# Kernel optimization log

Measured on AMD Instinct MI355X. Metric: run time of the kernel, lower is better.

Reference implementation:

```python
import math
import jax, jax.numpy as jnp
import numpy as np

B, S, HID = 2, 1024, 2048
H, D, R = 16, 128, 64            # heads, head_dim, rope_dim_per_head
KVC, QC = 512, 1536              # kv / query compressed dims
MAX_POS = 4096


def _lin(x, w, b):
    return x @ w.T + b


def _rotate_half(x):
    x1, x2 = x[..., : x.shape[-1] // 2], x[..., x.shape[-1] // 2 :]
    return jnp.concatenate([-x2, x1], axis=-1)


def _rope_tables(dim, end, theta=10000.0):
    freqs = 1.0 / (theta ** (jnp.arange(0, dim, 2)[: dim // 2].astype(jnp.float32) / dim))
    f = jnp.outer(jnp.arange(end, dtype=jnp.float32), freqs)  # [end, dim//2]
    cos, sin = jnp.cos(f), jnp.sin(f)
    # duplicate halves so tables broadcast against the full rope dim (standard HF convention)
    return jnp.concatenate([cos, cos], -1), jnp.concatenate([sin, sin], -1)


def setup_inputs() -> dict:
    key = jax.random.key(0)
    ks = jax.random.split(key, 17)
    w = lambda k, shape: (jax.random.normal(k, shape, jnp.float32) * 0.02)
    return {
        "hidden_states": jax.random.normal(ks[0], (B, S, HID), jnp.float32),
        "W_DKV_w": w(ks[1], (KVC, HID)),  "W_DKV_b": w(ks[2], (KVC,)),
        "W_UK_w":  w(ks[3], (H * D, KVC)), "W_UK_b":  w(ks[4], (H * D,)),
        "W_UV_w":  w(ks[5], (H * D, KVC)), "W_UV_b":  w(ks[6], (H * D,)),
        "W_KR_w":  w(ks[7], (R, D)),       "W_KR_b":  w(ks[8], (R,)),
        "W_DQ_w":  w(ks[9], (QC, HID)),    "W_DQ_b":  w(ks[10], (QC,)),
        "W_UQ_w":  w(ks[11], (H * D, QC)), "W_UQ_b":  w(ks[12], (H * D,)),
        "W_QR_w":  w(ks[13], (R, D)),      "W_QR_b":  w(ks[14], (R,)),
        "W_O_w":   w(ks[15], (HID, H * D)),"W_O_b":   w(ks[16], (HID,)),
    }


def reference(hidden_states, W_DKV_w, W_DKV_b, W_UK_w, W_UK_b, W_UV_w, W_UV_b,
              W_KR_w, W_KR_b, W_DQ_w, W_DQ_b, W_UQ_w, W_UQ_b,
              W_QR_w, W_QR_b, W_O_w, W_O_b):
    b, s = hidden_states.shape[:2]
    # latent KV compression + decompression
    c_kv = _lin(hidden_states, W_DKV_w, W_DKV_b)                      # [B,S,KVC]
    k = _lin(c_kv, W_UK_w, W_UK_b).reshape(b, s, H, D)
    v = _lin(c_kv, W_UV_w, W_UV_b).reshape(b, s, H, D)
    # latent Q compression + decompression
    c_q = _lin(hidden_states, W_DQ_w, W_DQ_b)                         # [B,S,QC]
    q = _lin(c_q, W_UQ_w, W_UQ_b).reshape(b, s, H, D)
    # decoupled rope sub-dims
    k_r = _lin(k, W_KR_w, W_KR_b)                                     # [B,S,H,R]
    q_r = _lin(q, W_QR_w, W_QR_b)                                     # [B,S,H,R]
    cos, sin = _rope_tables(R, MAX_POS)
    cos_p = cos[:s][:, None, :]                                       # [S,1,R] -> broadcast over B,H
    sin_p = sin[:s][:, None, :]
    q_r = q_r * cos_p + _rotate_half(q_r) * sin_p
    k_r = k_r * cos_p + _rotate_half(k_r) * sin_p
    # SDPA (no mask, no causal flag in original)
    scale = 1.0 / math.sqrt(D)
    scores = jnp.einsum("bqhd,bkhd->bhqk", q, k) * scale              # [B,H,S,S]
    probs = jax.nn.softmax(scores, axis=-1)
    attn = jnp.einsum("bhqk,bkhd->bqhd", probs, v).reshape(b, s, H * D)
    output = _lin(attn, W_O_w, W_O_b)                                 # [B,S,HID]
    return output, c_kv, k_r
```

## Files before the change

kernel.cpp:

```cpp
#include <hip/hip_runtime.h>
#include <cstdint>

typedef __bf16 bf16;
typedef __attribute__((ext_vector_type(8))) __bf16 bf16x8;
typedef __attribute__((ext_vector_type(4))) float f32x4;

#define MFMA16(a, b, c) __builtin_amdgcn_mfma_f32_16x16x32_bf16(a, b, c, 0, 0, 0)

__device__ __forceinline__ void async16(const bf16* g, bf16* l) {
  __builtin_amdgcn_global_load_lds(
      (const __attribute__((address_space(1))) void*)g,
      (__attribute__((address_space(3))) void*)l, 16, 0, 0);
}

__device__ __forceinline__ bf16x8 load8cvt(const float* p) {
  f32x4 a = *(const f32x4*)p;
  f32x4 b = *(const f32x4*)(p + 4);
  bf16x8 r;
  r[0] = (bf16)a[0]; r[1] = (bf16)a[1]; r[2] = (bf16)a[2]; r[3] = (bf16)a[3];
  r[4] = (bf16)b[0]; r[5] = (bf16)b[1]; r[6] = (bf16)b[2]; r[7] = (bf16)b[3];
  return r;
}

__global__ __launch_bounds__(256) void cvt_f32_bf16(const float* __restrict__ src,
                                                    bf16* __restrict__ dst, int n) {
  int i = (blockIdx.x * 256 + threadIdx.x) * 8;
  if (i >= n) return;
  *(bf16x8*)(dst + i) = load8cvt(src + i);
}

__global__ __launch_bounds__(256) void cvt6(
    const float* __restrict__ s0, bf16* __restrict__ d0, int n0,
    const float* __restrict__ s1, bf16* __restrict__ d1, int n1,
    const float* __restrict__ s2, bf16* __restrict__ d2, int n2,
    const float* __restrict__ s3, bf16* __restrict__ d3, int n3,
    const float* __restrict__ s4, bf16* __restrict__ d4, int n4,
    const float* __restrict__ s5, bf16* __restrict__ d5, int n5) {
  const float* s; bf16* d; int n;
  switch (blockIdx.y) {
    case 0: s = s0; d = d0; n = n0; break;
    case 1: s = s1; d = d1; n = n1; break;
    case 2: s = s2; d = d2; n = n2; break;
    case 3: s = s3; d = d3; n = n3; break;
    case 4: s = s4; d = d4; n = n4; break;
    default: s = s5; d = d5; n = n5; break;
  }
  int i = (blockIdx.x * 256 + threadIdx.x) * 8;
  if (i >= n) return;
  *(bf16x8*)(d + i) = load8cvt(s + i);
}

template <int MODE>
__global__ __launch_bounds__(256) void gemm_bb(
    const bf16* __restrict__ A, int lda,
    const bf16* __restrict__ Bm, int ldb,
    const float* __restrict__ bias0, const float* __restrict__ bias1, int nsplit,
    bf16* __restrict__ outb, float* __restrict__ outf, int ldo,
    int M, int N, int K) {
  __shared__ __align__(16) bf16 As[4][128 * 32];
  __shared__ __align__(16) bf16 Bs[4][64 * 32];
  const int t = threadIdx.x;
  const int lane = t & 63, w = t >> 6;
  const int quad = lane >> 4, l15 = lane & 15;

  const int nwg = gridDim.x * gridDim.y;
  const int id = blockIdx.y * gridDim.x + blockIdx.x;
  const int sw = (id & 7) * (nwg >> 3) + (id >> 3);
  const int bm = (sw / gridDim.x) * 128, bn = (sw % gridDim.x) * 64;

  const int wm = (w >> 1) * 64, wn = (w & 1) * 32;

  f32x4 acc[4][2] = {};

  const int srow = t >> 2;
  const int scol = (t & 3) * 8;
  const bf16* Ap = A + (int64_t)(bm + srow) * lda + scol;
  const bf16* Bp = Bm + (int64_t)(bn + srow) * ldb + scol;

  auto STAGE = [&](int buf, int k0) {
    async16(Ap + k0, &As[buf][w * 512]);
    async16(Ap + (int64_t)64 * lda + k0, &As[buf][2048 + w * 512]);
    async16(Bp + k0, &Bs[buf][w * 512]);
  };
  auto COMPUTE = [&](int buf) {
    bf16x8 a[4], bq[2];
#pragma unroll
    for (int mt = 0; mt < 4; ++mt)
      a[mt] = *(const bf16x8*)(&As[buf][(wm + mt * 16 + l15) * 32 + quad * 8]);
#pragma unroll
    for (int nt = 0; nt < 2; ++nt)
      bq[nt] = *(const bf16x8*)(&Bs[buf][(wn + nt * 16 + l15) * 32 + quad * 8]);
#pragma unroll
    for (int mt = 0; mt < 4; ++mt)
#pragma unroll
      for (int nt = 0; nt < 2; ++nt)
        acc[mt][nt] = MFMA16(a[mt], bq[nt], acc[mt][nt]);
  };

  const int K32 = K >> 5;
  STAGE(0, 0);
  STAGE(1, 32);
  STAGE(2, 64);
  for (int s = 0; s < K32; ++s) {
    if (s + 3 < K32) {
      STAGE((s + 3) & 3, (s + 3) << 5);
      asm volatile("s_waitcnt vmcnt(9)\n\ts_barrier" ::: "memory");
    } else {
      const int rem = K32 - 1 - s;
      if (rem >= 2)      asm volatile("s_waitcnt vmcnt(6)\n\ts_barrier" ::: "memory");
      else if (rem == 1) asm volatile("s_waitcnt vmcnt(3)\n\ts_barrier" ::: "memory");
      else               asm volatile("s_waitcnt vmcnt(0)\n\ts_barrier" ::: "memory");
    }
    COMPUTE(s & 3);
    asm volatile("s_waitcnt lgkmcnt(0)\n\ts_barrier" ::: "memory");
  }

  float bv[2];
#pragma unroll
  for (int nt = 0; nt < 2; ++nt) {
    int n = bn + wn + nt * 16 + l15;
    bv[nt] = (n < nsplit) ? bias0[n] : bias1[n - nsplit];
  }
#pragma unroll
  for (int mt = 0; mt < 4; ++mt)
#pragma unroll
    for (int nt = 0; nt < 2; ++nt)
#pragma unroll
      for (int r = 0; r < 4; ++r) {
        int64_t m = bm + wm + mt * 16 + quad * 4 + r;
        int n = bn + wn + nt * 16 + l15;
        float v = acc[mt][nt][r] + bv[nt];
        if (MODE != 1) outb[m * ldo + n] = (bf16)v;
        if (MODE == 1) outf[m * (int64_t)ldo + n] = v;
        if (MODE == 2 && n < nsplit) outf[m * nsplit + n] = v;
      }
}

__global__ __launch_bounds__(256) void kr_rope(const bf16* __restrict__ kmat,
                                               const float* __restrict__ Wkr,
                                               const float* __restrict__ bkr,
                                               float* __restrict__ krout) {
  const int t = threadIdx.x;
  const int lane = t & 63, w = t >> 6;
  const int quad = lane >> 4, l15 = lane & 15;
  const int row0 = blockIdx.x * 64 + w * 16;

  const int rr = row0 + l15;
  const bf16* krow = kmat + (int64_t)(rr >> 4) * 4096 + (rr & 15) * 128;
  bf16x8 af[4];
#pragma unroll
  for (int ks = 0; ks < 4; ++ks)
    af[ks] = *(const bf16x8*)(krow + ks * 32 + quad * 8);

  f32x4 acc[4] = {};
#pragma unroll
  for (int nt = 0; nt < 4; ++nt)
#pragma unroll
    for (int ks = 0; ks < 4; ++ks) {
      bf16x8 bf_ = load8cvt(Wkr + (nt * 16 + l15) * 128 + ks * 32 + quad * 8);
      acc[nt] = MFMA16(af[ks], bf_, acc[nt]);
    }

  float bv[4], fr[4];
#pragma unroll
  for (int nt = 0; nt < 4; ++nt) {
    bv[nt] = bkr[nt * 16 + l15];
    int j = ((nt & 1) * 16 + l15);
    fr[nt] = exp2f(-(float)j * 0.41524101186092034f);
  }

#pragma unroll
  for (int r = 0; r < 4; ++r) {
    int row = row0 + quad * 4 + r;
    int pos = (row >> 4) & 1023;
    float val[4];
#pragma unroll
    for (int nt = 0; nt < 4; ++nt) val[nt] = acc[nt][r] + bv[nt];
#pragma unroll
    for (int nt = 0; nt < 4; ++nt) {
      int n = nt * 16 + l15;
      float ang = (float)pos * fr[nt];
      float c = cosf(ang), s = sinf(ang);
      float partner = val[nt ^ 2];
      float o = val[nt] * c + ((nt < 2) ? -partner : partner) * s;
      krout[(int64_t)row * 64 + n] = o;
    }
  }
}

__global__ __launch_bounds__(256, 2) void attn_fwd(const bf16* __restrict__ q,
                                                   const bf16* __restrict__ k,
                                                   const bf16* __restrict__ v,
                                                   bf16* __restrict__ attn) {
  const int bh = blockIdx.x * 4 + (blockIdx.y >> 4);
  const int qt = blockIdx.y & 15;
  const int b = bh >> 4, h = bh & 15;
  __shared__ __align__(16) bf16 Kb[2][64 * 128];
  __shared__ __align__(16) bf16 Vt[128 * 72];
  __shared__ __align__(16) bf16 Pl[4][16 * 72];

  const int t = threadIdx.x;
  const int lane = t & 63, w = t >> 6;
  const int quad = lane >> 4, l15 = lane & 15;
  const int trow = b * 1024 + qt * 64 + w * 16;
  const float scale = 0.08838834764831845f;

  bf16x8 qf[4];
#pragma unroll
  for (int ks = 0; ks < 4; ++ks)
    qf[ks] = *(const bf16x8*)(q + (int64_t)(trow + l15) * 2048 + h * 128 +
                              ks * 32 + quad * 8);

  const bf16* kbase = k + (int64_t)b * 1024 * 4096 + h * 128;
  const int lrow = lane >> 4;
  int64_t koff[4];
#pragma unroll
  for (int c = 0; c < 4; ++c) {
    int row = w * 16 + c * 4 + lrow;
    koff[c] = (int64_t)row * 4096 + (((lane & 15) ^ (row & 7)) << 3);
  }

  const int skey = t >> 4;
  const int sd0 = (t & 15) * 8;
  const bf16* vp = v + (int64_t)b * 1024 * 4096 + h * 128 + sd0;

#pragma unroll
  for (int c = 0; c < 4; ++c)
    async16(kbase + koff[c], &Kb[0][w * 2048 + c * 512]);
  bf16x8 vreg[4];
#pragma unroll
  for (int r = 0; r < 4; ++r)
    vreg[r] = *(const bf16x8*)(vp + (int64_t)(r * 16 + skey) * 4096);

  f32x4 o[8] = {};
  float lrw[4] = {0.f, 0.f, 0.f, 0.f};

  for (int kt = 0; kt < 16; ++kt) {
    const int cur = kt & 1;
#pragma unroll
    for (int r = 0; r < 4; ++r) {
      int key = r * 16 + skey;
      int col = (((key >> 3) ^ ((sd0 >> 3) & 7)) << 3) + (key & 7);
#pragma unroll
      for (int j = 0; j < 8; ++j) Vt[(sd0 + j) * 72 + col] = vreg[r][j];
    }
    __syncthreads();

    if (kt + 1 < 16) {
      const bf16* kn = kbase + (int64_t)(kt + 1) * 64 * 4096;
#pragma unroll
      for (int c = 0; c < 4; ++c)
        async16(kn + koff[c], &Kb[cur ^ 1][w * 2048 + c * 512]);
#pragma unroll
      for (int r = 0; r < 4; ++r)
        vreg[r] = *(const bf16x8*)(vp + (int64_t)((kt + 1) * 64 + r * 16 + skey) * 4096);
    }

    f32x4 s[4] = {};
    __builtin_amdgcn_s_setprio(1);
#pragma unroll
    for (int nt = 0; nt < 4; ++nt)
#pragma unroll
      for (int ks = 0; ks < 4; ++ks) {
        int key = nt * 16 + l15;
        bf16x8 bfrg = *(const bf16x8*)(
            &Kb[cur][key * 128 + (((ks * 4 + quad) ^ (l15 & 7)) << 3)]);
        s[nt] = MFMA16(qf[ks], bfrg, s[nt]);
      }
    __builtin_amdgcn_s_setprio(0);

    float rsum[4] = {0.f, 0.f, 0.f, 0.f};
#pragma unroll
    for (int nt = 0; nt < 4; ++nt)
#pragma unroll
      for (int r = 0; r < 4; ++r) {
        float p = __expf(s[nt][r] * scale);
        rsum[r] += p;
        int row = quad * 4 + r;
        int blk = (nt * 2 + (l15 >> 3)) ^ (quad * 2 + (r >> 1));
        Pl[w][row * 72 + (blk << 3) + (l15 & 7)] = (bf16)p;
      }
#pragma unroll
    for (int r = 0; r < 4; ++r) lrw[r] += rsum[r];

    __builtin_amdgcn_s_setprio(1);
#pragma unroll
    for (int ks = 0; ks < 2; ++ks) {
      int ablk = (ks * 4 + quad) ^ (l15 >> 1);
      bf16x8 afrg = *(const bf16x8*)(&Pl[w][l15 * 72 + (ablk << 3)]);
#pragma unroll
      for (int dt = 0; dt < 8; ++dt) {
        int d = dt * 16 + l15;
        int kb = ((ks * 4 + quad) ^ ((d >> 3) & 7)) << 3;
        bf16x8 bfrg = *(const bf16x8*)(Vt + d * 72 + kb);
        o[dt] = MFMA16(afrg, bfrg, o[dt]);
      }
    }
    __builtin_amdgcn_s_setprio(0);
    asm volatile("s_waitcnt lgkmcnt(0)\n\ts_barrier" ::: "memory");
  }

  float inv[4];
#pragma unroll
  for (int r = 0; r < 4; ++r) {
    float ssum = lrw[r];
#pragma unroll
    for (int off = 8; off >= 1; off >>= 1) ssum += __shfl_xor(ssum, off, 64);
    inv[r] = 1.0f / ssum;
  }
#pragma unroll
  for (int dt = 0; dt < 8; ++dt)
#pragma unroll
    for (int r = 0; r < 4; ++r) {
      int64_t row = trow + quad * 4 + r;
      int col = h * 128 + dt * 16 + l15;
      attn[row * 2048 + col] = (bf16)(o[dt][r] * inv[r]);
    }
}

extern "C" void kernel_launch(void* const* d_in, const int* in_sizes, int n_in,
                              void* d_out, int out_size, void* d_ws, size_t ws_size,
                              hipStream_t stream) {
  const float* hidden = (const float*)d_in[0];
  const float* Wdkv = (const float*)d_in[1];
  const float* bdkv = (const float*)d_in[2];
  const float* Wuk  = (const float*)d_in[3];
  const float* buk  = (const float*)d_in[4];
  const float* Wuv  = (const float*)d_in[5];
  const float* buv  = (const float*)d_in[6];
  const float* Wkr  = (const float*)d_in[7];
  const float* bkr  = (const float*)d_in[8];
  const float* Wdq  = (const float*)d_in[9];
  const float* bdq  = (const float*)d_in[10];
  const float* Wuq  = (const float*)d_in[11];
  const float* buq  = (const float*)d_in[12];
  const float* Wo   = (const float*)d_in[15];
  const float* bo   = (const float*)d_in[16];

  float* out0 = (float*)d_out;
  float* c_kv = out0 + 4194304;
  float* k_r  = out0 + 5242880;

  bf16* DKVQ = (bf16*)d_ws;
  bf16* KV   = DKVQ + 4194304;

  bf16* WT   = KV;
  bf16* qx   = (bf16*)out0;
  bf16* hb   = qx + 4194304;
  bf16* WUKV = qx;
  bf16* Wuqb = hb;
  bf16* Wob  = (bf16*)k_r;

  cvt6<<<dim3(2048, 6), 256, 0, stream>>>(
      hidden, hb, 4194304,
      Wdkv, WT, 1048576,
      Wdq, WT + 1048576, 3145728,
      Wuk, WUKV, 1048576,
      Wuv, WUKV + 1048576, 1048576,
      Wo, Wob, 4194304);
  gemm_bb<2><<<dim3(32, 16), 256, 0, stream>>>(hb, 2048, WT, 2048, bdkv, bdq, 512,
                                               DKVQ, c_kv, 2048, 2048, 2048, 2048);
  cvt_f32_bf16<<<1536, 256, 0, stream>>>(Wuq, Wuqb, 3145728);
  gemm_bb<0><<<dim3(64, 16), 256, 0, stream>>>(DKVQ, 2048, WUKV, 512, buk, buv, 2048,
                                               KV, nullptr, 4096, 2048, 4096, 512);
  gemm_bb<0><<<dim3(32, 16), 256, 0, stream>>>(DKVQ + 512, 2048, Wuqb, 1536, buq, buq,
                                               2048, qx, nullptr, 2048, 2048, 2048, 1536);
  attn_fwd<<<dim3(8, 64), 256, 0, stream>>>(qx, KV, KV + 2048, DKVQ);
  gemm_bb<1><<<dim3(32, 16), 256, 0, stream>>>(DKVQ, 2048, Wob, 2048, bo, bo, 2048,
                                               nullptr, out0, 2048, 2048, 2048, 2048);
  kr_rope<<<512, 256, 0, stream>>>(KV, Wkr, bkr, k_r);
}
```

Before: 323.3 us.

## Emit V transposed from up-projection GEMM and use K=64 swizzled double-buffered tiles

The K/V up-projection GEMM now writes the V half transposed (head_dim-major, token-contiguous) through an LDS staging epilogue. This lets attention load V tiles with async global-to-LDS copies in a double-buffered pipeline instead of register loads followed by a scalar LDS transpose each iteration. The GEMM tile loop also switches from 4 stages of K=32 to 2 stages of K=64 with an XOR-swizzled LDS layout. The trade-offs are shallower prefetch in the GEMM, an extra LDS pass plus barrier in the V epilogue, and more LDS per attention block.

```diff
diff --git a/kernel.cpp b/kernel.cpp
--- a/kernel.cpp
+++ b/kernel.cpp
@@ -50,15 +50,15 @@
   *(bf16x8*)(d + i) = load8cvt(s + i);
 }
 
-template <int MODE>
+template <int MODE, bool TRANSV>
 __global__ __launch_bounds__(256) void gemm_bb(
     const bf16* __restrict__ A, int lda,
     const bf16* __restrict__ Bm, int ldb,
     const float* __restrict__ bias0, const float* __restrict__ bias1, int nsplit,
     bf16* __restrict__ outb, float* __restrict__ outf, int ldo,
     int M, int N, int K) {
-  __shared__ __align__(16) bf16 As[4][128 * 32];
-  __shared__ __align__(16) bf16 Bs[4][64 * 32];
+  __shared__ __align__(16) bf16 As[2][128 * 64];
+  __shared__ __align__(16) bf16 Bs[2][64 * 64];
   const int t = threadIdx.x;
   const int lane = t & 63, w = t >> 6;
   const int quad = lane >> 4, l15 = lane & 15;
@@ -72,46 +72,56 @@
 
   f32x4 acc[4][2] = {};
 
-  const int srow = t >> 2;
-  const int scol = (t & 3) * 8;
-  const bf16* Ap = A + (int64_t)(bm + srow) * lda + scol;
-  const bf16* Bp = Bm + (int64_t)(bn + srow) * ldb + scol;
+  const int r8 = lane >> 3;
+  const int sc = ((lane & 7) ^ (r8 & 7)) * 8;
+  const bf16* Ap = A + (int64_t)(bm + w * 32 + r8) * lda + sc;
+  const bf16* Bp = Bm + (int64_t)(bn + w * 16 + r8) * ldb + sc;
 
   auto STAGE = [&](int buf, int k0) {
-    async16(Ap + k0, &As[buf][w * 512]);
-    async16(Ap + (int64_t)64 * lda + k0, &As[buf][2048 + w * 512]);
-    async16(Bp + k0, &Bs[buf][w * 512]);
+#pragma unroll
+    for (int a = 0; a < 4; ++a)
+      async16(Ap + (int64_t)(a * 8) * lda + k0, &As[buf][(w * 32 + a * 8) * 64]);
+#pragma unroll
+    for (int bq = 0; bq < 2; ++bq)
+      async16(Bp + (int64_t)(bq * 8) * ldb + k0, &Bs[buf][(w * 16 + bq * 8) * 64]);
   };
   auto COMPUTE = [&](int buf) {
-    bf16x8 a[4], bq[2];
+    bf16x8 a[4][2], bb[2][2];
 #pragma unroll
     for (int mt = 0; mt < 4; ++mt)
-      a[mt] = *(const bf16x8*)(&As[buf][(wm + mt * 16 + l15) * 32 + quad * 8]);
+#pragma unroll
+      for (int ks = 0; ks < 2; ++ks) {
+        int row = wm + mt * 16 + l15;
+        a[mt][ks] = *(const bf16x8*)(
+            &As[buf][row * 64 + (((ks * 4 + quad) ^ (l15 & 7)) << 3)]);
+      }
 #pragma unroll
     for (int nt = 0; nt < 2; ++nt)
-      bq[nt] = *(const bf16x8*)(&Bs[buf][(wn + nt * 16 + l15) * 32 + quad * 8]);
-#pragma unroll
-    for (int mt = 0; mt < 4; ++mt)
-#pragma unroll
-      for (int nt = 0; nt < 2; ++nt)
-        acc[mt][nt] = MFMA16(a[mt], bq[nt], acc[mt][nt]);
+#pragma unroll
+      for (int ks = 0; ks < 2; ++ks) {
+        int row = wn + nt * 16 + l15;
+        bb[nt][ks] = *(const bf16x8*)(
+            &Bs[buf][row * 64 + (((ks * 4 + quad) ^ (l15 & 7)) << 3)]);
+      }
+#pragma unroll
+    for (int ks = 0; ks < 2; ++ks)
+#pragma unroll
+      for (int mt = 0; mt < 4; ++mt)
+#pragma unroll
+        for (int nt = 0; nt < 2; ++nt)
+          acc[mt][nt] = MFMA16(a[mt][ks], bb[nt][ks], acc[mt][nt]);
   };
 
-  const int K32 = K >> 5;
+  const int KS = K >> 6;
   STAGE(0, 0);
-  STAGE(1, 32);
-  STAGE(2, 64);
-  for (int s = 0; s < K32; ++s) {
-    if (s + 3 < K32) {
-      STAGE((s + 3) & 3, (s + 3) << 5);
-      asm volatile("s_waitcnt vmcnt(9)\n\ts_barrier" ::: "memory");
+  for (int s = 0; s < KS; ++s) {
+    if (s + 1 < KS) {
+      STAGE((s + 1) & 1, (s + 1) << 6);
+      asm volatile("s_waitcnt vmcnt(6)\n\ts_barrier" ::: "memory");
     } else {
-      const int rem = K32 - 1 - s;
-      if (rem >= 2)      asm volatile("s_waitcnt vmcnt(6)\n\ts_barrier" ::: "memory");
-      else if (rem == 1) asm volatile("s_waitcnt vmcnt(3)\n\ts_barrier" ::: "memory");
-      else               asm volatile("s_waitcnt vmcnt(0)\n\ts_barrier" ::: "memory");
-    }
-    COMPUTE(s & 3);
+      asm volatile("s_waitcnt vmcnt(0)\n\ts_barrier" ::: "memory");
+    }
+    COMPUTE(s & 1);
     asm volatile("s_waitcnt lgkmcnt(0)\n\ts_barrier" ::: "memory");
   }
 
@@ -121,6 +131,28 @@
     int n = bn + wn + nt * 16 + l15;
     bv[nt] = (n < nsplit) ? bias0[n] : bias1[n - nsplit];
   }
+
+  if (TRANSV && bn >= nsplit) {
+    bf16* Ls = (bf16*)As;
+#pragma unroll
+    for (int mt = 0; mt < 4; ++mt)
+#pragma unroll
+      for (int nt = 0; nt < 2; ++nt)
+#pragma unroll
+        for (int r = 0; r < 4; ++r)
+          Ls[(wn + nt * 16 + l15) * 136 + wm + mt * 16 + quad * 4 + r] =
+              (bf16)(acc[mt][nt][r] + bv[nt]);
+    __syncthreads();
+    const int rloc = t >> 2;
+    const int cb = (t & 3) * 32;
+#pragma unroll
+    for (int c = 0; c < 4; ++c) {
+      bf16x8 val = *(const bf16x8*)(Ls + rloc * 136 + cb + c * 8);
+      *(bf16x8*)(outb + (int64_t)(bn - nsplit + rloc) * ldo + nsplit + bm + cb + c * 8) = val;
+    }
+    return;
+  }
+
 #pragma unroll
   for (int mt = 0; mt < 4; ++mt)
 #pragma unroll
@@ -190,13 +222,13 @@
 
 __global__ __launch_bounds__(256, 2) void attn_fwd(const bf16* __restrict__ q,
                                                    const bf16* __restrict__ k,
-                                                   const bf16* __restrict__ v,
+                                                   const bf16* __restrict__ vt,
                                                    bf16* __restrict__ attn) {
   const int bh = blockIdx.x * 4 + (blockIdx.y >> 4);
   const int qt = blockIdx.y & 15;
   const int b = bh >> 4, h = bh & 15;
   __shared__ __align__(16) bf16 Kb[2][64 * 128];
-  __shared__ __align__(16) bf16 Vt[128 * 72];
+  __shared__ __align__(16) bf16 Vb[2][128 * 64];
   __shared__ __align__(16) bf16 Pl[4][16 * 72];
 
   const int t = threadIdx.x;
@@ -212,48 +244,40 @@
                               ks * 32 + quad * 8);
 
   const bf16* kbase = k + (int64_t)b * 1024 * 4096 + h * 128;
-  const int lrow = lane >> 4;
+  const int lr4 = lane >> 4;
   int64_t koff[4];
 #pragma unroll
   for (int c = 0; c < 4; ++c) {
-    int row = w * 16 + c * 4 + lrow;
+    int row = w * 16 + c * 4 + lr4;
     koff[c] = (int64_t)row * 4096 + (((lane & 15) ^ (row & 7)) << 3);
   }
 
-  const int skey = t >> 4;
-  const int sd0 = (t & 15) * 8;
-  const bf16* vp = v + (int64_t)b * 1024 * 4096 + h * 128 + sd0;
-
-#pragma unroll
-  for (int c = 0; c < 4; ++c)
-    async16(kbase + koff[c], &Kb[0][w * 2048 + c * 512]);
-  bf16x8 vreg[4];
-#pragma unroll
-  for (int r = 0; r < 4; ++r)
-    vreg[r] = *(const bf16x8*)(vp + (int64_t)(r * 16 + skey) * 4096);
-
+  const int r8 = lane >> 3;
+  const int vsc = ((lane & 7) ^ (r8 & 7)) * 8;
+  const bf16* Vp = vt + (int64_t)(h * 128 + w * 32 + r8) * 4096 + b * 1024 + vsc;
+
+  auto STAGE = [&](int buf, int kt) {
+    const bf16* kn = kbase + (int64_t)kt * 64 * 4096;
+#pragma unroll
+    for (int c = 0; c < 4; ++c)
+      async16(kn + koff[c], &Kb[buf][(w * 16 + c * 4) * 128]);
+    const bf16* vn = Vp + kt * 64;
+#pragma unroll
+    for (int a = 0; a < 4; ++a)
+      async16(vn + (int64_t)(a * 8) * 4096, &Vb[buf][(w * 32 + a * 8) * 64]);
+  };
+
+  STAGE(0, 0);
   f32x4 o[8] = {};
   float lrw[4] = {0.f, 0.f, 0.f, 0.f};
 
   for (int kt = 0; kt < 16; ++kt) {
     const int cur = kt & 1;
-#pragma unroll
-    for (int r = 0; r < 4; ++r) {
-      int key = r * 16 + skey;
-      int col = (((key >> 3) ^ ((sd0 >> 3) & 7)) << 3) + (key & 7);
-#pragma unroll
-      for (int j = 0; j < 8; ++j) Vt[(sd0 + j) * 72 + col] = vreg[r][j];
-    }
-    __syncthreads();
-
     if (kt + 1 < 16) {
-      const bf16* kn = kbase + (int64_t)(kt + 1) * 64 * 4096;
-#pragma unroll
-      for (int c = 0; c < 4; ++c)
-        async16(kn + koff[c], &Kb[cur ^ 1][w * 2048 + c * 512]);
-#pragma unroll
-      for (int r = 0; r < 4; ++r)
-        vreg[r] = *(const bf16x8*)(vp + (int64_t)((kt + 1) * 64 + r * 16 + skey) * 4096);
+      STAGE(cur ^ 1, kt + 1);
+      asm volatile("s_waitcnt vmcnt(8)\n\ts_barrier" ::: "memory");
+    } else {
+      asm volatile("s_waitcnt vmcnt(0)\n\ts_barrier" ::: "memory");
     }
 
     f32x4 s[4] = {};
@@ -291,8 +315,8 @@
 #pragma unroll
       for (int dt = 0; dt < 8; ++dt) {
         int d = dt * 16 + l15;
-        int kb = ((ks * 4 + quad) ^ ((d >> 3) & 7)) << 3;
-        bf16x8 bfrg = *(const bf16x8*)(Vt + d * 72 + kb);
+        bf16x8 bfrg = *(const bf16x8*)(
+            &Vb[cur][d * 64 + (((ks * 4 + quad) ^ (l15 & 7)) << 3)]);
         o[dt] = MFMA16(afrg, bfrg, o[dt]);
       }
     }
@@ -358,15 +382,15 @@
       Wuk, WUKV, 1048576,
       Wuv, WUKV + 1048576, 1048576,
       Wo, Wob, 4194304);
-  gemm_bb<2><<<dim3(32, 16), 256, 0, stream>>>(hb, 2048, WT, 2048, bdkv, bdq, 512,
-                                               DKVQ, c_kv, 2048, 2048, 2048, 2048);
+  gemm_bb<2, false><<<dim3(32, 16), 256, 0, stream>>>(
+      hb, 2048, WT, 2048, bdkv, bdq, 512, DKVQ, c_kv, 2048, 2048, 2048, 2048);
   cvt_f32_bf16<<<1536, 256, 0, stream>>>(Wuq, Wuqb, 3145728);
-  gemm_bb<0><<<dim3(64, 16), 256, 0, stream>>>(DKVQ, 2048, WUKV, 512, buk, buv, 2048,
-                                               KV, nullptr, 4096, 2048, 4096, 512);
-  gemm_bb<0><<<dim3(32, 16), 256, 0, stream>>>(DKVQ + 512, 2048, Wuqb, 1536, buq, buq,
-                                               2048, qx, nullptr, 2048, 2048, 2048, 1536);
+  gemm_bb<0, true><<<dim3(64, 16), 256, 0, stream>>>(
+      DKVQ, 2048, WUKV, 512, buk, buv, 2048, KV, nullptr, 4096, 2048, 4096, 512);
+  gemm_bb<0, false><<<dim3(32, 16), 256, 0, stream>>>(
+      DKVQ + 512, 2048, Wuqb, 1536, buq, buq, 2048, qx, nullptr, 2048, 2048, 2048, 1536);
   attn_fwd<<<dim3(8, 64), 256, 0, stream>>>(qx, KV, KV + 2048, DKVQ);
-  gemm_bb<1><<<dim3(32, 16), 256, 0, stream>>>(DKVQ, 2048, Wob, 2048, bo, bo, 2048,
-                                               nullptr, out0, 2048, 2048, 2048, 2048);
+  gemm_bb<1, false><<<dim3(32, 16), 256, 0, stream>>>(
+      DKVQ, 2048, Wob, 2048, bo, bo, 2048, nullptr, out0, 2048, 2048, 2048, 2048);
   kr_rope<<<512, 256, 0, stream>>>(KV, Wkr, bkr, k_r);
 }
```

Measured after the change: 284.7 us. 11.9% less time.
